# Performance work log

Measured on AMD Instinct MI355X. Metric: run time of the kernel, lower is better.

## Reference

```python
import jax, jax.numpy as jnp
import numpy as np

DIM = 768
NUM_HEADS = 12
HEAD_DIM = DIM // NUM_HEADS
SCALE = HEAD_DIM ** -0.5


def setup_inputs() -> dict:
    key = jax.random.key(0)
    k_x, k_qkv, k_proj, k_pb = jax.random.split(key, 4)
    B, N = 8, 1024
    x = jax.random.normal(k_x, (B, N, DIM), dtype=jnp.float32)
    # nn.Linear(dim, 3*dim, bias=False): weight [3*dim, dim]
    w_qkv = jax.random.normal(k_qkv, (3 * DIM, DIM), dtype=jnp.float32) * (DIM ** -0.5)
    # nn.Linear(dim, dim): weight [dim, dim], bias [dim]
    w_proj = jax.random.normal(k_proj, (DIM, DIM), dtype=jnp.float32) * (DIM ** -0.5)
    b_proj = jax.random.normal(k_pb, (DIM,), dtype=jnp.float32) * 0.01
    return {"x": x, "w_qkv": w_qkv, "w_proj": w_proj, "b_proj": b_proj}


def reference(x, w_qkv, w_proj, b_proj):
    B, N, C = x.shape
    H, D = NUM_HEADS, HEAD_DIM
    # qkv: [B, N, 3C] -> [3, B, H, N, D]
    qkv = jnp.einsum('bnc,oc->bno', x, w_qkv)
    qkv = qkv.reshape(B, N, 3, H, D).transpose(2, 0, 3, 1, 4)
    q, k, v = qkv[0], qkv[1], qkv[2]
    # scores in float32 (module explicitly casts to float)
    attn = jnp.einsum('bhnd,bhmd->bhnm', q.astype(jnp.float32), k.astype(jnp.float32)) * SCALE
    attn = jax.nn.softmax(attn, axis=-1)
    attn = jnp.where(jnp.isnan(attn), 0.0, attn)  # masked_fill nan -> 0
    out = jnp.einsum('bhnm,bhmd->bhnd', attn, v.astype(jnp.float32))
    out = out.transpose(0, 2, 1, 3).reshape(B, N, C)
    out = jnp.einsum('bnc,oc->bno', out, w_proj) + b_proj
    return out
```

## Files before the change

### kernel.cpp

```cpp
#include <hip/hip_runtime.h>

typedef _Float16 half8 __attribute__((ext_vector_type(8)));
typedef _Float16 half4 __attribute__((ext_vector_type(4)));
typedef float f32x4 __attribute__((ext_vector_type(4)));

#define NHEAD 12
#define HDIM  64
#define SEQ   1024
#define CDIM  768
#define O3    2304
#define MTOK  8192

__device__ __forceinline__ void load_lds16(const void* g, void* l) {
  __builtin_amdgcn_global_load_lds(
      (const __attribute__((address_space(1))) unsigned int*)g,
      (__attribute__((address_space(3))) unsigned int*)l, 16, 0, 0);
}

__global__ __launch_bounds__(256) void cast_f2h(const float* __restrict__ in,
                                                _Float16* __restrict__ out) {
  size_t i = ((size_t)blockIdx.x * 256 + threadIdx.x) * 4;
  float4 v = *reinterpret_cast<const float4*>(in + i);
  half4 h;
  h[0] = (_Float16)v.x; h[1] = (_Float16)v.y; h[2] = (_Float16)v.z; h[3] = (_Float16)v.w;
  *reinterpret_cast<half4*>(out + i) = h;
}

__global__ __launch_bounds__(256) void qkv_gemm(const _Float16* __restrict__ A,
                                                const _Float16* __restrict__ Bw,
                                                _Float16* __restrict__ Qh,
                                                _Float16* __restrict__ Kh,
                                                _Float16* __restrict__ VT) {
  __shared__ _Float16 As[128 * 32];
  __shared__ _Float16 Bs[128 * 32];
  const int tid  = threadIdx.x;
  const int lane = tid & 63;
  const int wv   = tid >> 6;
  const int wm   = wv >> 1;
  const int wn   = wv & 1;
  const int fr   = lane & 15;
  const int kg   = lane >> 4;
  const int m0   = blockIdx.y * 128;
  const int n0   = blockIdx.x * 128;

  f32x4 acc[4][4];
#pragma unroll
  for (int i = 0; i < 4; ++i)
#pragma unroll
    for (int j = 0; j < 4; ++j) acc[i][j] = (f32x4){0.f, 0.f, 0.f, 0.f};

  for (int kt = 0; kt < CDIM; kt += 32) {
#pragma unroll
    for (int r = 0; r < 2; ++r) {
      const int c = r * 256 + tid;
      const int row = c >> 2, cc = c & 3;
      load_lds16(A + (size_t)(m0 + row) * CDIM + kt + ((cc ^ (row & 3)) * 8), &As[c * 8]);
    }
#pragma unroll
    for (int r = 0; r < 2; ++r) {
      const int c = r * 256 + tid;
      const int row = c >> 2, cc = c & 3;
      load_lds16(Bw + (size_t)(n0 + row) * CDIM + kt + ((cc ^ (row & 3)) * 8), &Bs[c * 8]);
    }
    __syncthreads();
    half8 a[4], b[4];
#pragma unroll
    for (int i = 0; i < 4; ++i) {
      const int row = wm * 64 + i * 16 + fr;
      a[i] = *reinterpret_cast<half8*>(&As[row * 32 + ((kg ^ (row & 3)) * 8)]);
    }
#pragma unroll
    for (int j = 0; j < 4; ++j) {
      const int row = wn * 64 + j * 16 + fr;
      b[j] = *reinterpret_cast<half8*>(&Bs[row * 32 + ((kg ^ (row & 3)) * 8)]);
    }
#pragma unroll
    for (int i = 0; i < 4; ++i)
#pragma unroll
      for (int j = 0; j < 4; ++j)
        acc[i][j] = __builtin_amdgcn_mfma_f32_16x16x32_f16(a[i], b[j], acc[i][j], 0, 0, 0);
    __syncthreads();
  }

#pragma unroll
  for (int i = 0; i < 4; ++i) {
    const int mrow = m0 + wm * 64 + i * 16 + (lane >> 4) * 4;
#pragma unroll
    for (int j = 0; j < 4; ++j) {
      const int ocol = n0 + wn * 64 + j * 16 + fr;
      const int t  = ocol / CDIM;
      const int hd = ocol - t * CDIM;
      const int h  = hd >> 6, d = hd & 63;
#pragma unroll
      for (int r = 0; r < 4; ++r) {
        const int m  = mrow + r;
        const int bb = m >> 10, nn = m & 1023;
        const float v = acc[i][j][r];
        if (t == 0)
          Qh[(((size_t)bb * NHEAD + h) * SEQ + nn) * HDIM + d] = (_Float16)(v * 0.125f);
        else if (t == 1)
          Kh[(((size_t)bb * NHEAD + h) * SEQ + nn) * HDIM + d] = (_Float16)v;
        else
          VT[(((size_t)bb * NHEAD + h) * HDIM + d) * SEQ + nn] = (_Float16)v;
      }
    }
  }
}

__global__ __launch_bounds__(256) void attn_kernel(const _Float16* __restrict__ Qh,
                                                   const _Float16* __restrict__ Kh,
                                                   const _Float16* __restrict__ VT,
                                                   _Float16* __restrict__ AO) {
  __shared__ _Float16 Ks[64 * 64];
  __shared__ _Float16 Vs[64 * 64];
  __shared__ _Float16 Ps[4 * 16 * 64];
  const int tid  = threadIdx.x;
  const int lane = tid & 63;
  const int w    = tid >> 6;
  const int fr   = lane & 15;
  const int kg   = lane >> 4;
  const int kh   = kg * 8;
  const int bh   = blockIdx.x;
  const int qt   = blockIdx.y;
  const int q0   = qt * 64 + w * 16;
  const size_t qkbase = (size_t)bh * SEQ * HDIM;
  char* const psw = (char*)&Ps[w * 16 * 64];

  half8 qb[2];
#pragma unroll
  for (int ks = 0; ks < 2; ++ks)
    qb[ks] = *reinterpret_cast<const half8*>(
        &Qh[qkbase + (size_t)(q0 + fr) * HDIM + ks * 32 + kh]);

  f32x4 O[4];
  float mrun = -__builtin_inff();
  float lrun = 0.f;
#pragma unroll
  for (int fd = 0; fd < 4; ++fd) O[fd] = (f32x4){0.f, 0.f, 0.f, 0.f};

  for (int kt = 0; kt < SEQ; kt += 64) {
    __syncthreads();
#pragma unroll
    for (int r = 0; r < 2; ++r) {
      const int c = r * 256 + tid;
      const int row = c >> 3, cc = c & 7;
      load_lds16(&Kh[qkbase + (size_t)(kt + row) * HDIM + ((cc ^ (row & 7)) * 8)], &Ks[c * 8]);
    }
#pragma unroll
    for (int r = 0; r < 2; ++r) {
      const int c = r * 256 + tid;
      const int row = c >> 3, cc = c & 7;
      load_lds16(&VT[(size_t)bh * HDIM * SEQ + (size_t)row * SEQ + kt + ((cc ^ (row & 7)) * 8)],
                 &Vs[c * 8]);
    }
    __syncthreads();

    f32x4 st[4];
#pragma unroll
    for (int fc = 0; fc < 4; ++fc) st[fc] = (f32x4){0.f, 0.f, 0.f, 0.f};
#pragma unroll
    for (int ks = 0; ks < 2; ++ks) {
#pragma unroll
      for (int fc = 0; fc < 4; ++fc) {
        const int row = fc * 16 + fr;
        const int colh = ks * 32 + kh;
        half8 ka = *reinterpret_cast<half8*>(&Ks[row * 64 + (((colh >> 3) ^ (row & 7)) << 3)]);
        st[fc] = __builtin_amdgcn_mfma_f32_16x16x32_f16(ka, qb[ks], st[fc], 0, 0, 0);
      }
    }

    float mx = st[0][0];
#pragma unroll
    for (int fc = 0; fc < 4; ++fc)
#pragma unroll
      for (int r = 0; r < 4; ++r) mx = fmaxf(mx, st[fc][r]);
    mx = fmaxf(mx, __shfl_xor(mx, 16));
    mx = fmaxf(mx, __shfl_xor(mx, 32));
    const float mnew = fmaxf(mrun, mx);
    const float corr = __expf(mrun - mnew);
    mrun = mnew;
    float rs = 0.f;
#pragma unroll
    for (int fc = 0; fc < 4; ++fc)
#pragma unroll
      for (int r = 0; r < 4; ++r) {
        const float p = __expf(st[fc][r] - mnew);
        st[fc][r] = p;
        rs += p;
      }
    rs += __shfl_xor(rs, 16);
    rs += __shfl_xor(rs, 32);
    lrun = lrun * corr + rs;

#pragma unroll
    for (int r = 0; r < 4; ++r) {
      const float c4 = __shfl(corr, kg * 4 + r);
#pragma unroll
      for (int fd = 0; fd < 4; ++fd) O[fd][r] *= c4;
    }

#pragma unroll
    for (int fc = 0; fc < 4; ++fc) {
      half4 pk;
      pk[0] = (_Float16)st[fc][0];
      pk[1] = (_Float16)st[fc][1];
      pk[2] = (_Float16)st[fc][2];
      pk[3] = (_Float16)st[fc][3];
      const int slot = (fc * 2 + (kg >> 1)) ^ (fr & 7);
      *reinterpret_cast<half4*>(psw + fr * 128 + slot * 16 + (kg & 1) * 8) = pk;
    }

#pragma unroll
    for (int ks = 0; ks < 2; ++ks) {
      const int rslot = (ks * 4 + kg) ^ (fr & 7);
      half8 pa = *reinterpret_cast<half8*>(psw + fr * 128 + rslot * 16);
#pragma unroll
      for (int fd = 0; fd < 4; ++fd) {
        const int row = fd * 16 + fr;
        const int colh = ks * 32 + kh;
        half8 vb = *reinterpret_cast<half8*>(&Vs[row * 64 + (((colh >> 3) ^ (row & 7)) << 3)]);
        O[fd] = __builtin_amdgcn_mfma_f32_16x16x32_f16(pa, vb, O[fd], 0, 0, 0);
      }
    }
  }

  const int b = bh / NHEAD, h = bh % NHEAD;
  const float linv = 1.0f / lrun;
#pragma unroll
  for (int r = 0; r < 4; ++r) {
    const float lq = __shfl(linv, kg * 4 + r);
    const int n = q0 + kg * 4 + r;
#pragma unroll
    for (int fd = 0; fd < 4; ++fd)
      AO[((size_t)b * SEQ + n) * CDIM + h * HDIM + fd * 16 + fr] =
          (_Float16)(O[fd][r] * lq);
  }
}

__global__ __launch_bounds__(256) void proj_gemm(const _Float16* __restrict__ A,
                                                 const _Float16* __restrict__ Bw,
                                                 const float* __restrict__ bias,
                                                 float* __restrict__ Out) {
  __shared__ _Float16 As[128 * 32];
  __shared__ _Float16 Bs[128 * 32];
  const int tid  = threadIdx.x;
  const int lane = tid & 63;
  const int wv   = tid >> 6;
  const int wm   = wv >> 1;
  const int wn   = wv & 1;
  const int fr   = lane & 15;
  const int kg   = lane >> 4;
  const int m0   = blockIdx.y * 128;
  const int n0   = blockIdx.x * 128;

  f32x4 acc[4][4];
#pragma unroll
  for (int i = 0; i < 4; ++i)
#pragma unroll
    for (int j = 0; j < 4; ++j) acc[i][j] = (f32x4){0.f, 0.f, 0.f, 0.f};

  for (int kt = 0; kt < CDIM; kt += 32) {
#pragma unroll
    for (int r = 0; r < 2; ++r) {
      const int c = r * 256 + tid;
      const int row = c >> 2, cc = c & 3;
      load_lds16(A + (size_t)(m0 + row) * CDIM + kt + ((cc ^ (row & 3)) * 8), &As[c * 8]);
    }
#pragma unroll
    for (int r = 0; r < 2; ++r) {
      const int c = r * 256 + tid;
      const int row = c >> 2, cc = c & 3;
      load_lds16(Bw + (size_t)(n0 + row) * CDIM + kt + ((cc ^ (row & 3)) * 8), &Bs[c * 8]);
    }
    __syncthreads();
    half8 a[4], b[4];
#pragma unroll
    for (int i = 0; i < 4; ++i) {
      const int row = wm * 64 + i * 16 + fr;
      a[i] = *reinterpret_cast<half8*>(&As[row * 32 + ((kg ^ (row & 3)) * 8)]);
    }
#pragma unroll
    for (int j = 0; j < 4; ++j) {
      const int row = wn * 64 + j * 16 + fr;
      b[j] = *reinterpret_cast<half8*>(&Bs[row * 32 + ((kg ^ (row & 3)) * 8)]);
    }
#pragma unroll
    for (int i = 0; i < 4; ++i)
#pragma unroll
      for (int j = 0; j < 4; ++j)
        acc[i][j] = __builtin_amdgcn_mfma_f32_16x16x32_f16(a[i], b[j], acc[i][j], 0, 0, 0);
    __syncthreads();
  }

#pragma unroll
  for (int i = 0; i < 4; ++i) {
    const int mrow = m0 + wm * 64 + i * 16 + (lane >> 4) * 4;
#pragma unroll
    for (int j = 0; j < 4; ++j) {
      const int ocol = n0 + wn * 64 + j * 16 + fr;
      const float bv = bias[ocol];
#pragma unroll
      for (int r = 0; r < 4; ++r)
        Out[(size_t)(mrow + r) * CDIM + ocol] = acc[i][j][r] + bv;
    }
  }
}

extern "C" void kernel_launch(void* const* d_in, const int* in_sizes, int n_in,
                              void* d_out, int out_size, void* d_ws, size_t ws_size,
                              hipStream_t stream) {
  const float* x     = (const float*)d_in[0];
  const float* wqkv  = (const float*)d_in[1];
  const float* wproj = (const float*)d_in[2];
  const float* bproj = (const float*)d_in[3];
  float* out = (float*)d_out;

  char* ws = (char*)d_ws;
  _Float16* x_h     = (_Float16*)(ws);
  _Float16* wqkv_h  = (_Float16*)(ws + 12582912);
  _Float16* wproj_h = (_Float16*)(ws + 16121856);
  _Float16* Qh      = (_Float16*)(ws + 17301504);
  _Float16* Kh      = (_Float16*)(ws + 29884416);
  _Float16* VT      = (_Float16*)(ws + 42467328);
  _Float16* AOh     = (_Float16*)(ws + 55050240);

  cast_f2h<<<6291456 / 1024, 256, 0, stream>>>(x, x_h);
  cast_f2h<<<1769472 / 1024, 256, 0, stream>>>(wqkv, wqkv_h);
  cast_f2h<<<589824 / 1024, 256, 0, stream>>>(wproj, wproj_h);

  qkv_gemm<<<dim3(O3 / 128, MTOK / 128), 256, 0, stream>>>(x_h, wqkv_h, Qh, Kh, VT);
  attn_kernel<<<dim3(96, 16), 256, 0, stream>>>(Qh, Kh, VT, AOh);
  proj_gemm<<<dim3(CDIM / 128, MTOK / 128), 256, 0, stream>>>(AOh, wproj_h, bproj, out);
}
```

Measured before the change: 160.8 us.

## Double-buffer LDS tiles and swizzle block order in QKV and proj GEMMs

Both GEMM kernels now keep two LDS stages and issue the global-to-LDS loads for the next K tile before computing on the current one, with one barrier per iteration instead of two. Block indices are remapped in groups of eight, intended to improve L2 reuse across neighbouring blocks. The QKV epilogue hoists the q/k/v selector to once per block and uses shift-based addressing. This doubles LDS use per block, which may lower occupancy. It also assumes the grid is divisible by 8 and has 18 (QKV) or 6 (proj) column tiles.

New measurement: 164.9 us. 2.6% more time.

```diff
diff --git a/kernel.cpp b/kernel.cpp
--- a/kernel.cpp
+++ b/kernel.cpp
@@ -31,8 +31,8 @@
                                                 _Float16* __restrict__ Qh,
                                                 _Float16* __restrict__ Kh,
                                                 _Float16* __restrict__ VT) {
-  __shared__ _Float16 As[128 * 32];
-  __shared__ _Float16 Bs[128 * 32];
+  __shared__ _Float16 As[2][128 * 32];
+  __shared__ _Float16 Bs[2][128 * 32];
   const int tid  = threadIdx.x;
   const int lane = tid & 63;
   const int wv   = tid >> 6;
@@ -40,8 +40,12 @@
   const int wn   = wv & 1;
   const int fr   = lane & 15;
   const int kg   = lane >> 4;
-  const int m0   = blockIdx.y * 128;
-  const int n0   = blockIdx.x * 128;
+
+  const int lin = blockIdx.y * gridDim.x + blockIdx.x;
+  const int cpx = (gridDim.x * gridDim.y) >> 3;
+  const int swz = (lin & 7) * cpx + (lin >> 3);
+  const int m0  = (swz / 18) * 128;
+  const int n0  = (swz % 18) * 128;
 
   f32x4 acc[4][4];
 #pragma unroll
@@ -49,47 +53,59 @@
 #pragma unroll
     for (int j = 0; j < 4; ++j) acc[i][j] = (f32x4){0.f, 0.f, 0.f, 0.f};
 
-  for (int kt = 0; kt < CDIM; kt += 32) {
+  auto stage = [&](int buf, int kt) {
 #pragma unroll
     for (int r = 0; r < 2; ++r) {
       const int c = r * 256 + tid;
       const int row = c >> 2, cc = c & 3;
-      load_lds16(A + (size_t)(m0 + row) * CDIM + kt + ((cc ^ (row & 3)) * 8), &As[c * 8]);
+      load_lds16(A + (size_t)(m0 + row) * CDIM + kt + ((cc ^ (row & 3)) * 8),
+                 &As[buf][c * 8]);
     }
 #pragma unroll
     for (int r = 0; r < 2; ++r) {
       const int c = r * 256 + tid;
       const int row = c >> 2, cc = c & 3;
-      load_lds16(Bw + (size_t)(n0 + row) * CDIM + kt + ((cc ^ (row & 3)) * 8), &Bs[c * 8]);
-    }
-    __syncthreads();
+      load_lds16(Bw + (size_t)(n0 + row) * CDIM + kt + ((cc ^ (row & 3)) * 8),
+                 &Bs[buf][c * 8]);
+    }
+  };
+
+  int cur = 0;
+  stage(0, 0);
+  __syncthreads();
+
+  for (int it = 0; it < 24; ++it) {
+    if (it + 1 < 24) stage(cur ^ 1, (it + 1) * 32);
     half8 a[4], b[4];
 #pragma unroll
     for (int i = 0; i < 4; ++i) {
       const int row = wm * 64 + i * 16 + fr;
-      a[i] = *reinterpret_cast<half8*>(&As[row * 32 + ((kg ^ (row & 3)) * 8)]);
+      a[i] = *reinterpret_cast<half8*>(&As[cur][row * 32 + ((kg ^ (row & 3)) * 8)]);
     }
 #pragma unroll
     for (int j = 0; j < 4; ++j) {
       const int row = wn * 64 + j * 16 + fr;
-      b[j] = *reinterpret_cast<half8*>(&Bs[row * 32 + ((kg ^ (row & 3)) * 8)]);
+      b[j] = *reinterpret_cast<half8*>(&Bs[cur][row * 32 + ((kg ^ (row & 3)) * 8)]);
     }
 #pragma unroll
     for (int i = 0; i < 4; ++i)
 #pragma unroll
       for (int j = 0; j < 4; ++j)
         acc[i][j] = __builtin_amdgcn_mfma_f32_16x16x32_f16(a[i], b[j], acc[i][j], 0, 0, 0);
-    __syncthreads();
-  }
-
+    if (it + 1 < 24) {
+      __syncthreads();
+      cur ^= 1;
+    }
+  }
+
+  const int t     = n0 / CDIM;
+  const int hbase = n0 - t * CDIM;
 #pragma unroll
   for (int i = 0; i < 4; ++i) {
-    const int mrow = m0 + wm * 64 + i * 16 + (lane >> 4) * 4;
+    const int mrow = m0 + wm * 64 + i * 16 + kg * 4;
 #pragma unroll
     for (int j = 0; j < 4; ++j) {
-      const int ocol = n0 + wn * 64 + j * 16 + fr;
-      const int t  = ocol / CDIM;
-      const int hd = ocol - t * CDIM;
+      const int hd = hbase + wn * 64 + j * 16 + fr;
       const int h  = hd >> 6, d = hd & 63;
 #pragma unroll
       for (int r = 0; r < 4; ++r) {
@@ -97,11 +113,11 @@
         const int bb = m >> 10, nn = m & 1023;
         const float v = acc[i][j][r];
         if (t == 0)
-          Qh[(((size_t)bb * NHEAD + h) * SEQ + nn) * HDIM + d] = (_Float16)(v * 0.125f);
+          Qh[(((size_t)(bb * NHEAD + h)) << 16) + (nn << 6) + d] = (_Float16)(v * 0.125f);
         else if (t == 1)
-          Kh[(((size_t)bb * NHEAD + h) * SEQ + nn) * HDIM + d] = (_Float16)v;
+          Kh[(((size_t)(bb * NHEAD + h)) << 16) + (nn << 6) + d] = (_Float16)v;
         else
-          VT[(((size_t)bb * NHEAD + h) * HDIM + d) * SEQ + nn] = (_Float16)v;
+          VT[(((size_t)(bb * NHEAD + h)) << 16) + (d << 10) + nn] = (_Float16)v;
       }
     }
   }
@@ -241,8 +257,8 @@
                                                  const _Float16* __restrict__ Bw,
                                                  const float* __restrict__ bias,
                                                  float* __restrict__ Out) {
-  __shared__ _Float16 As[128 * 32];
-  __shared__ _Float16 Bs[128 * 32];
+  __shared__ _Float16 As[2][128 * 32];
+  __shared__ _Float16 Bs[2][128 * 32];
   const int tid  = threadIdx.x;
   const int lane = tid & 63;
   const int wv   = tid >> 6;
@@ -250,8 +266,12 @@
   const int wn   = wv & 1;
   const int fr   = lane & 15;
   const int kg   = lane >> 4;
-  const int m0   = blockIdx.y * 128;
-  const int n0   = blockIdx.x * 128;
+
+  const int lin = blockIdx.y * gridDim.x + blockIdx.x;
+  const int cpx = (gridDim.x * gridDim.y) >> 3;
+  const int swz = (lin & 7) * cpx + (lin >> 3);
+  const int m0  = (swz / 6) * 128;
+  const int n0  = (swz % 6) * 128;
 
   f32x4 acc[4][4];
 #pragma unroll
@@ -259,42 +279,54 @@
 #pragma unroll
     for (int j = 0; j < 4; ++j) acc[i][j] = (f32x4){0.f, 0.f, 0.f, 0.f};
 
-  for (int kt = 0; kt < CDIM; kt += 32) {
+  auto stage = [&](int buf, int kt) {
 #pragma unroll
     for (int r = 0; r < 2; ++r) {
       const int c = r * 256 + tid;
       const int row = c >> 2, cc = c & 3;
-      load_lds16(A + (size_t)(m0 + row) * CDIM + kt + ((cc ^ (row & 3)) * 8), &As[c * 8]);
+      load_lds16(A + (size_t)(m0 + row) * CDIM + kt + ((cc ^ (row & 3)) * 8),
+                 &As[buf][c * 8]);
     }
 #pragma unroll
     for (int r = 0; r < 2; ++r) {
       const int c = r * 256 + tid;
       const int row = c >> 2, cc = c & 3;
-      load_lds16(Bw + (size_t)(n0 + row) * CDIM + kt + ((cc ^ (row & 3)) * 8), &Bs[c * 8]);
-    }
-    __syncthreads();
+      load_lds16(Bw + (size_t)(n0 + row) * CDIM + kt + ((cc ^ (row & 3)) * 8),
+                 &Bs[buf][c * 8]);
+    }
+  };
+
+  int cur = 0;
+  stage(0, 0);
+  __syncthreads();
+
+  for (int it = 0; it < 24; ++it) {
+    if (it + 1 < 24) stage(cur ^ 1, (it + 1) * 32);
     half8 a[4], b[4];
 #pragma unroll
     for (int i = 0; i < 4; ++i) {
       const int row = wm * 64 + i * 16 + fr;
-      a[i] = *reinterpret_cast<half8*>(&As[row * 32 + ((kg ^ (row & 3)) * 8)]);
+      a[i] = *reinterpret_cast<half8*>(&As[cur][row * 32 + ((kg ^ (row & 3)) * 8)]);
     }
 #pragma unroll
     for (int j = 0; j < 4; ++j) {
       const int row = wn * 64 + j * 16 + fr;
-      b[j] = *reinterpret_cast<half8*>(&Bs[row * 32 + ((kg ^ (row & 3)) * 8)]);
+      b[j] = *reinterpret_cast<half8*>(&Bs[cur][row * 32 + ((kg ^ (row & 3)) * 8)]);
     }
 #pragma unroll
     for (int i = 0; i < 4; ++i)
 #pragma unroll
       for (int j = 0; j < 4; ++j)
         acc[i][j] = __builtin_amdgcn_mfma_f32_16x16x32_f16(a[i], b[j], acc[i][j], 0, 0, 0);
-    __syncthreads();
+    if (it + 1 < 24) {
+      __syncthreads();
+      cur ^= 1;
+    }
   }
 
 #pragma unroll
   for (int i = 0; i < 4; ++i) {
-    const int mrow = m0 + wm * 64 + i * 16 + (lane >> 4) * 4;
+    const int mrow = m0 + wm * 64 + i * 16 + kg * 4;
 #pragma unroll
     for (int j = 0; j < 4; ++j) {
       const int ocol = n0 + wn * 64 + j * 16 + fr;
```
